# Kernel tuning notes

Measured on AMD Instinct MI355X. Metric: run time of the kernel, lower is better.

The kernel has to match this reference:

```python
import jax, jax.numpy as jnp
import numpy as np

D = 33        # n_vertices
HID = 256     # hidden_features
N_RANKS = 5


def setup_inputs() -> dict:
    key = jax.random.key(0)
    ks = jax.random.split(key, 8)
    img = jax.random.uniform(ks[0], (1, 3, 2160, 3840), dtype=jnp.float32)
    param = jax.random.normal(ks[1], (1, N_RANKS), dtype=jnp.float32) * 0.1

    def lin(k, fan_in, fan_out):
        lim = 1.0 / np.sqrt(fan_in)
        kw, kb = jax.random.split(k)
        W = jax.random.uniform(kw, (fan_in, fan_out), minval=-lim, maxval=lim, dtype=jnp.float32)
        b = jax.random.uniform(kb, (fan_out,), minval=-lim, maxval=lim, dtype=jnp.float32)
        return W, b

    W0, b0 = lin(ks[2], 11, HID)
    W1, b1 = lin(ks[3], HID, HID)
    W2, b2 = lin(ks[4], HID, HID)
    W3, b3 = lin(ks[5], HID, HID)
    W4, b4 = lin(ks[6], HID, 3)
    return dict(img=img, param=param, W0=W0, b0=b0, W1=W1, b1=b1,
                W2=W2, b2=b2, W3=W3, b3=b3, W4=W4, b4=b4)


def _identity_lut_flat():
    # torch: stack(meshgrid(ij), 0)/ (D-1), flip(0), reshape (1,3,D^3)
    v = jnp.arange(D, dtype=jnp.float32)
    g = jnp.stack(jnp.meshgrid(v, v, v, indexing='ij'), axis=0) / (D - 1)
    return g[::-1].reshape(1, 3, -1)  # (1, 3, 35937)


def _nilut(intensity, W0, b0, W1, b1, W2, b2, W3, b3, W4, b4):
    # intensity: (B, N, 8) = [r, g, b, params...]
    inp = jnp.concatenate([intensity, jnp.sort(intensity[..., :3], axis=-1)], axis=-1)  # (B,N,11)
    zero_inp = inp[:1].at[:, :, 3:-3].set(0.0)  # zero the param channels

    def net(x):
        h = jax.nn.relu(x @ W0 + b0)
        h = jnp.tanh(h @ W1 + b1)
        h = jnp.tanh(h @ W2 + b2)
        h = jnp.tanh(h @ W3 + b3)
        return h @ W4 + b4

    return net(inp) - net(zero_inp) + intensity[..., :3]


def _trilinear_lookup(img, luts):
    # img: (B,3,H,W) in [0,1]; luts: (B,3,D,D,D) indexed [c, b_idx, g_idx, r_idx]
    s = img * (D - 1)
    idx = jnp.clip(jnp.floor(s), 0, D - 2).astype(jnp.int32)
    f = s - idx.astype(s.dtype)

    def one(lut_b, idx_b, f_b):
        ir, ig, ib = idx_b[0], idx_b[1], idx_b[2]
        fr, fg, fb = f_b[0], f_b[1], f_b[2]

        def g(db, dg, dr):
            return lut_b[:, ib + db, ig + dg, ir + dr]  # (3,H,W)

        return (g(0, 0, 0) * (1 - fb) * (1 - fg) * (1 - fr)
                + g(0, 0, 1) * (1 - fb) * (1 - fg) * fr
                + g(0, 1, 0) * (1 - fb) * fg * (1 - fr)
                + g(0, 1, 1) * (1 - fb) * fg * fr
                + g(1, 0, 0) * fb * (1 - fg) * (1 - fr)
                + g(1, 0, 1) * fb * (1 - fg) * fr
                + g(1, 1, 0) * fb * fg * (1 - fr)
                + g(1, 1, 1) * fb * fg * fr)

    return jax.vmap(one)(luts, idx, f)


def reference(img, param, W0, b0, W1, b1, W2, b2, W3, b3, W4, b4):
    B = param.shape[0]
    ident = _identity_lut_flat()                              # (1,3,N)
    Nl = ident.shape[2]
    tiled = jnp.broadcast_to(param[:, :, None], (B, N_RANKS, Nl))
    ins = jnp.concatenate([jnp.broadcast_to(ident, (B, 3, Nl)), tiled], axis=1)  # (B,8,N)
    ins = jnp.transpose(ins, (0, 2, 1))                       # (B,N,8)
    luts = _nilut(ins, W0, b0, W1, b1, W2, b2, W3, b3, W4, b4)  # (B,N,3)
    luts = jnp.transpose(luts, (0, 2, 1)).reshape(B, 3, D, D, D)
    img_rep = jnp.broadcast_to(img, (B,) + img.shape[1:])
    return _trilinear_lookup(img_rep, luts)
```

## Files before the change

kernel.cpp:

```cpp
#include <hip/hip_runtime.h>
#include <hip/hip_fp16.h>
#include <math.h>

#define NPTS 35937
#define HID 256
#define TPB 256

typedef __attribute__((ext_vector_type(8))) short short8;
typedef __attribute__((ext_vector_type(4))) float f32x4;

__device__ __forceinline__ float fast_tanh(float x) {
    float e = __expf(2.0f * x);
    return 1.0f - __fdividef(2.0f, e + 1.0f);
}

__device__ __forceinline__ short f2bf(float f) {
    union { float f; unsigned u; } v; v.f = f;
    unsigned r = (v.u + 0x7fffu + ((v.u >> 16) & 1u)) >> 16;
    return (short)r;
}

__device__ __forceinline__ unsigned cvt_pk_bf16(float a, float b) {
    unsigned r;
    asm("v_cvt_pk_bf16_f32 %0, %1, %2" : "=v"(r) : "v"(a), "v"(b));
    return r;
}

#define W1P_OFF 8192
#define W2P_OFF 73728
#define W3P_OFF 139264
#define W4P_OFF 204800
#define LUT_BYTE_OFF 417792
#define CELL_BYTE_OFF 992896

__global__ __launch_bounds__(256) void pack_weights_kernel(
    const float* __restrict__ W0, const float* __restrict__ W1,
    const float* __restrict__ W2, const float* __restrict__ W3,
    const float* __restrict__ W4, short* __restrict__ P)
{
    int id = blockIdx.x * 256 + threadIdx.x;
    if (id >= 26112) return;
    const float* W; int f, NT, KREAL, NROW; long pbase;
    if (id < 1024)       { W = W0; f = id;         NT = 16; KREAL = 11;  NROW = 256; pbase = 0; }
    else if (id < 9216)  { W = W1; f = id - 1024;  NT = 16; KREAL = 256; NROW = 256; pbase = W1P_OFF; }
    else if (id < 17408) { W = W2; f = id - 9216;  NT = 16; KREAL = 256; NROW = 256; pbase = W2P_OFF; }
    else if (id < 25600) { W = W3; f = id - 17408; NT = 16; KREAL = 256; NROW = 256; pbase = W3P_OFF; }
    else                 { W = W4; f = id - 25600; NT = 1;  KREAL = 256; NROW = 3;   pbase = W4P_OFF; }
    int lane = f & 63;
    int tile = f >> 6;
    int nt = tile % NT, kt = tile / NT;
    int n  = nt * 16 + (lane & 15);
    int k0 = kt * 32 + ((lane >> 4) & 3) * 8;
    short v[8];
    #pragma unroll
    for (int j = 0; j < 8; ++j) {
        int k = k0 + j;
        float x = (k < KREAL && n < NROW) ? W[k * NROW + n] : 0.0f;
        v[j] = f2bf(x);
    }
    *(short8*)(P + pbase + (long)f * 8) = *(short8*)v;
}

#define HSTR 264

__global__ __launch_bounds__(256) void nilut_mfma_kernel(
    const float* __restrict__ param, const short* __restrict__ P,
    const float* __restrict__ b0, const float* __restrict__ b1,
    const float* __restrict__ b2, const float* __restrict__ b3,
    const float* __restrict__ b4, float* __restrict__ lut4)
{
    __shared__ short Hs[32][HSTR];
    __shared__ short Is[32][40];
    __shared__ float OB[32][4];

    const int t = threadIdx.x;
    const int pblock = blockIdx.x * 16;
    const int lane = t & 63;
    const int wid  = t >> 6;
    const int lr = lane & 15;
    const int hi = lane >> 4;
    const int k8 = hi * 8;

    if (t < 32) {
        int pn = pblock + (t >> 1);
        if (pn >= NPTS) pn = NPTS - 1;
        int v = t & 1;
        int ii = pn / 1089;
        int rem = pn - ii * 1089;
        int jj = rem / 33;
        int kk = rem - jj * 33;
        float r = kk * (1.0f / 32.0f);
        float g = jj * (1.0f / 32.0f);
        float b = ii * (1.0f / 32.0f);
        float lo = fminf(r, fminf(g, b));
        float hv = fmaxf(r, fmaxf(g, b));
        float mid = r + g + b - lo - hv;
        Is[t][0] = f2bf(r); Is[t][1] = f2bf(g); Is[t][2] = f2bf(b);
        #pragma unroll
        for (int q = 0; q < 5; ++q)
            Is[t][3 + q] = (v == 0) ? f2bf(param[q]) : (short)0;
        Is[t][8] = f2bf(lo); Is[t][9] = f2bf(mid); Is[t][10] = f2bf(hv);
        #pragma unroll
        for (int q = 11; q < 40; ++q) Is[t][q] = (short)0;
    }
    __syncthreads();

    f32x4 acc[2][4];
    const int nbase = wid * 64 + hi * 4;

    {
        #pragma unroll
        for (int c = 0; c < 4; ++c) {
            float4 bv = *(const float4*)(b0 + nbase + c * 16);
            f32x4 in = {bv.x, bv.y, bv.z, bv.w};
            #pragma unroll
            for (int rt = 0; rt < 2; ++rt) acc[rt][c] = in;
        }
        short8 a[2], bfr[4];
        #pragma unroll
        for (int rt = 0; rt < 2; ++rt) a[rt] = *(const short8*)&Is[rt * 16 + lr][k8];
        #pragma unroll
        for (int c = 0; c < 4; ++c)
            bfr[c] = *(const short8*)(P + ((long)(wid * 4 + c) * 64 + lane) * 8);
        #pragma unroll
        for (int rt = 0; rt < 2; ++rt)
            #pragma unroll
            for (int c = 0; c < 4; ++c)
                acc[rt][c] = __builtin_amdgcn_mfma_f32_16x16x32_bf16(bfr[c], a[rt], acc[rt][c], 0, 0, 0);
        #pragma unroll
        for (int rt = 0; rt < 2; ++rt)
            #pragma unroll
            for (int c = 0; c < 4; ++c) {
                uint2 w;
                w.x = cvt_pk_bf16(fmaxf(acc[rt][c][0], 0.0f), fmaxf(acc[rt][c][1], 0.0f));
                w.y = cvt_pk_bf16(fmaxf(acc[rt][c][2], 0.0f), fmaxf(acc[rt][c][3], 0.0f));
                *(uint2*)&Hs[rt * 16 + lr][nbase + c * 16] = w;
            }
    }
    __syncthreads();

    const long loff[3] = {W1P_OFF, W2P_OFF, W3P_OFF};
    const float* bptr[3];
    bptr[0] = b1; bptr[1] = b2; bptr[2] = b3;
    for (int L = 0; L < 3; ++L) {
        const short* WL = P + loff[L];
        const float* bb = bptr[L];
        #pragma unroll
        for (int c = 0; c < 4; ++c) {
            float4 bv = *(const float4*)(bb + nbase + c * 16);
            f32x4 in = {bv.x, bv.y, bv.z, bv.w};
            #pragma unroll
            for (int rt = 0; rt < 2; ++rt) acc[rt][c] = in;
        }
        #pragma unroll
        for (int kt = 0; kt < 8; ++kt) {
            short8 a[2], bfr[4];
            #pragma unroll
            for (int rt = 0; rt < 2; ++rt)
                a[rt] = *(const short8*)&Hs[rt * 16 + lr][kt * 32 + k8];
            #pragma unroll
            for (int c = 0; c < 4; ++c)
                bfr[c] = *(const short8*)(WL + ((long)(kt * 16 + wid * 4 + c) * 64 + lane) * 8);
            #pragma unroll
            for (int rt = 0; rt < 2; ++rt)
                #pragma unroll
                for (int c = 0; c < 4; ++c)
                    acc[rt][c] = __builtin_amdgcn_mfma_f32_16x16x32_bf16(bfr[c], a[rt], acc[rt][c], 0, 0, 0);
        }
        __syncthreads();
        #pragma unroll
        for (int rt = 0; rt < 2; ++rt)
            #pragma unroll
            for (int c = 0; c < 4; ++c) {
                uint2 w;
                w.x = cvt_pk_bf16(fast_tanh(acc[rt][c][0]), fast_tanh(acc[rt][c][1]));
                w.y = cvt_pk_bf16(fast_tanh(acc[rt][c][2]), fast_tanh(acc[rt][c][3]));
                *(uint2*)&Hs[rt * 16 + lr][nbase + c * 16] = w;
            }
        __syncthreads();
    }

    if (wid < 2) {
        float bv = (lr < 3) ? b4[lr] : 0.0f;
        f32x4 a4 = {bv, bv, bv, bv};
        const short* WL = P + W4P_OFF;
        #pragma unroll
        for (int kt = 0; kt < 8; ++kt) {
            short8 a = *(const short8*)&Hs[wid * 16 + lr][kt * 32 + k8];
            short8 b = *(const short8*)(WL + ((long)kt * 64 + lane) * 8);
            a4 = __builtin_amdgcn_mfma_f32_16x16x32_bf16(a, b, a4, 0, 0, 0);
        }
        if (lr < 3) {
            #pragma unroll
            for (int q = 0; q < 4; ++q)
                OB[wid * 16 + hi * 4 + q][lr] = a4[q];
        }
    }
    __syncthreads();

    if (t < 48) {
        int pl = t / 3, c = t - pl * 3;
        int n = pblock + pl;
        if (n < NPTS) {
            int ii = n / 1089;
            int rem = n - ii * 1089;
            int jj = rem / 33;
            int kk = rem - jj * 33;
            float rgb = (c == 0) ? kk * (1.0f / 32.0f)
                      : (c == 1) ? jj * (1.0f / 32.0f)
                                 : ii * (1.0f / 32.0f);
            lut4[n * 4 + c] = OB[2 * pl][c] - OB[2 * pl + 1][c] + rgb;
        }
    }
}

__global__ __launch_bounds__(256) void expand_cells_kernel(
    const float* __restrict__ lut4, __half* __restrict__ cells)
{
    int id = blockIdx.x * 256 + threadIdx.x;
    if (id >= 32768 * 8) return;
    int corner = id & 7;
    int cell   = id >> 3;
    int ir = cell & 31, ig = (cell >> 5) & 31, ib = cell >> 10;
    int dr = corner & 1, dg = (corner >> 1) & 1, db = (corner >> 2) & 1;
    int src = (ib + db) * 1089 + (ig + dg) * 33 + (ir + dr);
    float4 v = *(const float4*)(lut4 + (long)src * 4);
    union { __half h[4]; uint2 u; } pk;
    pk.h[0] = __float2half_rn(v.x);
    pk.h[1] = __float2half_rn(v.y);
    pk.h[2] = __float2half_rn(v.z);
    pk.h[3] = __float2half_rn(0.0f);
    *(uint2*)(cells + (long)cell * 32 + corner * 4) = pk.u;
}

#define LERP(a, b, f) fmaf((f), (b) - (a), (a))

__global__ __launch_bounds__(256) void apply_lut_kernel(
    const float* __restrict__ img, const __half* __restrict__ cells,
    float* __restrict__ out)
{
    const int NP = 2160 * 3840;
    int idx = blockIdx.x * blockDim.x + threadIdx.x;
    int p = idx * 4;
    if (p >= NP) return;

    float4 rv = *(const float4*)(img + p);
    float4 gv = *(const float4*)(img + NP + p);
    float4 bv = *(const float4*)(img + 2 * NP + p);

    float rr[4] = {rv.x, rv.y, rv.z, rv.w};
    float gg[4] = {gv.x, gv.y, gv.z, gv.w};
    float bb[4] = {bv.x, bv.y, bv.z, bv.w};
    float ox[4], oy[4], oz[4];

    #pragma unroll
    for (int u = 0; u < 4; ++u) {
        float sr = rr[u] * 32.0f, sg = gg[u] * 32.0f, sb = bb[u] * 32.0f;
        float fir = fminf(fmaxf(floorf(sr), 0.0f), 31.0f);
        float fig = fminf(fmaxf(floorf(sg), 0.0f), 31.0f);
        float fib = fminf(fmaxf(floorf(sb), 0.0f), 31.0f);
        float fr = sr - fir, fg = sg - fig, fb = sb - fib;
        int ir = (int)fir, ig = (int)fig, ib = (int)fib;

        const short8* cb = (const short8*)(cells + ((long)(ib * 1024 + ig * 32 + ir)) * 32);
        union { short8 s; __half h[8]; } u0, u1, u2, u3;
        u0.s = cb[0]; u1.s = cb[1]; u2.s = cb[2]; u3.s = cb[3];

        float v00[3], v01[3], v10[3], v11[3];
        #pragma unroll
        for (int c = 0; c < 3; ++c) {
            v00[c] = LERP(__half2float(u0.h[c]), __half2float(u0.h[c + 4]), fr);
            v01[c] = LERP(__half2float(u1.h[c]), __half2float(u1.h[c + 4]), fr);
            v10[c] = LERP(__half2float(u2.h[c]), __half2float(u2.h[c + 4]), fr);
            v11[c] = LERP(__half2float(u3.h[c]), __half2float(u3.h[c + 4]), fr);
        }
        ox[u] = LERP(LERP(v00[0], v01[0], fg), LERP(v10[0], v11[0], fg), fb);
        oy[u] = LERP(LERP(v00[1], v01[1], fg), LERP(v10[1], v11[1], fg), fb);
        oz[u] = LERP(LERP(v00[2], v01[2], fg), LERP(v10[2], v11[2], fg), fb);
    }

    *(float4*)(out + p)          = make_float4(ox[0], ox[1], ox[2], ox[3]);
    *(float4*)(out + NP + p)     = make_float4(oy[0], oy[1], oy[2], oy[3]);
    *(float4*)(out + 2 * NP + p) = make_float4(oz[0], oz[1], oz[2], oz[3]);
}

extern "C" void kernel_launch(void* const* d_in, const int* in_sizes, int n_in,
                              void* d_out, int out_size, void* d_ws, size_t ws_size,
                              hipStream_t stream) {
    const float* img   = (const float*)d_in[0];
    const float* param = (const float*)d_in[1];
    const float* W0 = (const float*)d_in[2];
    const float* b0 = (const float*)d_in[3];
    const float* W1 = (const float*)d_in[4];
    const float* b1 = (const float*)d_in[5];
    const float* W2 = (const float*)d_in[6];
    const float* b2 = (const float*)d_in[7];
    const float* W3 = (const float*)d_in[8];
    const float* b3 = (const float*)d_in[9];
    const float* W4 = (const float*)d_in[10];
    const float* b4 = (const float*)d_in[11];

    short*  P     = (short*)d_ws;
    float*  lut4  = (float*)((char*)d_ws + LUT_BYTE_OFF);
    __half* cells = (__half*)((char*)d_ws + CELL_BYTE_OFF);
    float*  out   = (float*)d_out;

    hipLaunchKernelGGL(pack_weights_kernel, dim3(102), dim3(TPB), 0, stream,
                       W0, W1, W2, W3, W4, P);

    int lut_blocks = (NPTS + 15) / 16;
    hipLaunchKernelGGL(nilut_mfma_kernel, dim3(lut_blocks), dim3(TPB), 0, stream,
                       param, P, b0, b1, b2, b3, b4, lut4);

    hipLaunchKernelGGL(expand_cells_kernel, dim3(1024), dim3(TPB), 0, stream,
                       lut4, cells);

    const int NP = 2160 * 3840;
    int apply_blocks = (NP / 4 + TPB - 1) / TPB;
    hipLaunchKernelGGL(apply_lut_kernel, dim3(apply_blocks), dim3(TPB), 0, stream,
                       img, cells, out);
}
```

Baseline: 132.4 us.

## Fuse cell expansion into NILUT kernel and make apply kernel grid-stride with prefetch

The NILUT kernel now scatters each LUT vertex directly as fp16 into the eight cells it belongs to. This removes the intermediate lut4 buffer and the separate expand_cells launch. The apply kernel becomes a persistent grid-stride loop over 2048 blocks that prefetches the next quad's image data while processing the current one. Costs are scattered 8-byte stores from only 16 threads per block, and lower parallelism in the apply stage.

```diff
diff --git a/kernel.cpp b/kernel.cpp
--- a/kernel.cpp
+++ b/kernel.cpp
@@ -30,7 +30,6 @@
 #define W2P_OFF 73728
 #define W3P_OFF 139264
 #define W4P_OFF 204800
-#define LUT_BYTE_OFF 417792
 #define CELL_BYTE_OFF 992896
 
 __global__ __launch_bounds__(256) void pack_weights_kernel(
@@ -67,7 +66,7 @@
     const float* __restrict__ param, const short* __restrict__ P,
     const float* __restrict__ b0, const float* __restrict__ b1,
     const float* __restrict__ b2, const float* __restrict__ b3,
-    const float* __restrict__ b4, float* __restrict__ lut4)
+    const float* __restrict__ b4, __half* __restrict__ cells)
 {
     __shared__ short Hs[32][HSTR];
     __shared__ short Is[32][40];
@@ -198,90 +197,103 @@
     }
     __syncthreads();
 
-    if (t < 48) {
-        int pl = t / 3, c = t - pl * 3;
-        int n = pblock + pl;
+    if (t < 16) {
+        int n = pblock + t;
         if (n < NPTS) {
             int ii = n / 1089;
             int rem = n - ii * 1089;
             int jj = rem / 33;
             int kk = rem - jj * 33;
-            float rgb = (c == 0) ? kk * (1.0f / 32.0f)
-                      : (c == 1) ? jj * (1.0f / 32.0f)
-                                 : ii * (1.0f / 32.0f);
-            lut4[n * 4 + c] = OB[2 * pl][c] - OB[2 * pl + 1][c] + rgb;
-        }
-    }
-}
-
-__global__ __launch_bounds__(256) void expand_cells_kernel(
-    const float* __restrict__ lut4, __half* __restrict__ cells)
+            float vr = OB[2 * t][0] - OB[2 * t + 1][0] + kk * (1.0f / 32.0f);
+            float vg = OB[2 * t][1] - OB[2 * t + 1][1] + jj * (1.0f / 32.0f);
+            float vb = OB[2 * t][2] - OB[2 * t + 1][2] + ii * (1.0f / 32.0f);
+            union { __half h[4]; uint2 u; } pk;
+            pk.h[0] = __float2half_rn(vr);
+            pk.h[1] = __float2half_rn(vg);
+            pk.h[2] = __float2half_rn(vb);
+            pk.h[3] = __float2half_rn(0.0f);
+            #pragma unroll
+            for (int corner = 0; corner < 8; ++corner) {
+                int dr = corner & 1, dg = (corner >> 1) & 1, db = corner >> 2;
+                int cr = kk - dr, cg = jj - dg, cb = ii - db;
+                if ((unsigned)cr < 32u && (unsigned)cg < 32u && (unsigned)cb < 32u) {
+                    long cell = cb * 1024 + cg * 32 + cr;
+                    *(uint2*)(cells + cell * 32 + corner * 4) = pk.u;
+                }
+            }
+        }
+    }
+}
+
+#define LERP(a, b, f) fmaf((f), (b) - (a), (a))
+#define AP_BLOCKS 2048
+#define AP_TPB 256
+
+__device__ __forceinline__ void lut_px(const __half* __restrict__ cells,
+                                       float r, float g, float b,
+                                       float& orr, float& og, float& ob)
 {
-    int id = blockIdx.x * 256 + threadIdx.x;
-    if (id >= 32768 * 8) return;
-    int corner = id & 7;
-    int cell   = id >> 3;
-    int ir = cell & 31, ig = (cell >> 5) & 31, ib = cell >> 10;
-    int dr = corner & 1, dg = (corner >> 1) & 1, db = (corner >> 2) & 1;
-    int src = (ib + db) * 1089 + (ig + dg) * 33 + (ir + dr);
-    float4 v = *(const float4*)(lut4 + (long)src * 4);
-    union { __half h[4]; uint2 u; } pk;
-    pk.h[0] = __float2half_rn(v.x);
-    pk.h[1] = __float2half_rn(v.y);
-    pk.h[2] = __float2half_rn(v.z);
-    pk.h[3] = __float2half_rn(0.0f);
-    *(uint2*)(cells + (long)cell * 32 + corner * 4) = pk.u;
-}
-
-#define LERP(a, b, f) fmaf((f), (b) - (a), (a))
+    float sr = r * 32.0f, sg = g * 32.0f, sb = b * 32.0f;
+    float fir = fminf(fmaxf(floorf(sr), 0.0f), 31.0f);
+    float fig = fminf(fmaxf(floorf(sg), 0.0f), 31.0f);
+    float fib = fminf(fmaxf(floorf(sb), 0.0f), 31.0f);
+    float fr = sr - fir, fg = sg - fig, fb = sb - fib;
+    int ir = (int)fir, ig = (int)fig, ib = (int)fib;
+
+    const short8* cb = (const short8*)(cells + ((long)(ib * 1024 + ig * 32 + ir)) * 32);
+    union { short8 s; __half h[8]; } u0, u1, u2, u3;
+    u0.s = cb[0]; u1.s = cb[1]; u2.s = cb[2]; u3.s = cb[3];
+
+    float v00[3], v01[3], v10[3], v11[3];
+    #pragma unroll
+    for (int c = 0; c < 3; ++c) {
+        v00[c] = LERP(__half2float(u0.h[c]), __half2float(u0.h[c + 4]), fr);
+        v01[c] = LERP(__half2float(u1.h[c]), __half2float(u1.h[c + 4]), fr);
+        v10[c] = LERP(__half2float(u2.h[c]), __half2float(u2.h[c + 4]), fr);
+        v11[c] = LERP(__half2float(u3.h[c]), __half2float(u3.h[c + 4]), fr);
+    }
+    orr = LERP(LERP(v00[0], v01[0], fg), LERP(v10[0], v11[0], fg), fb);
+    og  = LERP(LERP(v00[1], v01[1], fg), LERP(v10[1], v11[1], fg), fb);
+    ob  = LERP(LERP(v00[2], v01[2], fg), LERP(v10[2], v11[2], fg), fb);
+}
 
 __global__ __launch_bounds__(256) void apply_lut_kernel(
     const float* __restrict__ img, const __half* __restrict__ cells,
     float* __restrict__ out)
 {
     const int NP = 2160 * 3840;
-    int idx = blockIdx.x * blockDim.x + threadIdx.x;
-    int p = idx * 4;
-    if (p >= NP) return;
-
-    float4 rv = *(const float4*)(img + p);
-    float4 gv = *(const float4*)(img + NP + p);
-    float4 bv = *(const float4*)(img + 2 * NP + p);
-
-    float rr[4] = {rv.x, rv.y, rv.z, rv.w};
-    float gg[4] = {gv.x, gv.y, gv.z, gv.w};
-    float bb[4] = {bv.x, bv.y, bv.z, bv.w};
-    float ox[4], oy[4], oz[4];
-
-    #pragma unroll
-    for (int u = 0; u < 4; ++u) {
-        float sr = rr[u] * 32.0f, sg = gg[u] * 32.0f, sb = bb[u] * 32.0f;
-        float fir = fminf(fmaxf(floorf(sr), 0.0f), 31.0f);
-        float fig = fminf(fmaxf(floorf(sg), 0.0f), 31.0f);
-        float fib = fminf(fmaxf(floorf(sb), 0.0f), 31.0f);
-        float fr = sr - fir, fg = sg - fig, fb = sb - fib;
-        int ir = (int)fir, ig = (int)fig, ib = (int)fib;
-
-        const short8* cb = (const short8*)(cells + ((long)(ib * 1024 + ig * 32 + ir)) * 32);
-        union { short8 s; __half h[8]; } u0, u1, u2, u3;
-        u0.s = cb[0]; u1.s = cb[1]; u2.s = cb[2]; u3.s = cb[3];
-
-        float v00[3], v01[3], v10[3], v11[3];
-        #pragma unroll
-        for (int c = 0; c < 3; ++c) {
-            v00[c] = LERP(__half2float(u0.h[c]), __half2float(u0.h[c + 4]), fr);
-            v01[c] = LERP(__half2float(u1.h[c]), __half2float(u1.h[c + 4]), fr);
-            v10[c] = LERP(__half2float(u2.h[c]), __half2float(u2.h[c + 4]), fr);
-            v11[c] = LERP(__half2float(u3.h[c]), __half2float(u3.h[c + 4]), fr);
-        }
-        ox[u] = LERP(LERP(v00[0], v01[0], fg), LERP(v10[0], v11[0], fg), fb);
-        oy[u] = LERP(LERP(v00[1], v01[1], fg), LERP(v10[1], v11[1], fg), fb);
-        oz[u] = LERP(LERP(v00[2], v01[2], fg), LERP(v10[2], v11[2], fg), fb);
-    }
-
-    *(float4*)(out + p)          = make_float4(ox[0], ox[1], ox[2], ox[3]);
-    *(float4*)(out + NP + p)     = make_float4(oy[0], oy[1], oy[2], oy[3]);
-    *(float4*)(out + 2 * NP + p) = make_float4(oz[0], oz[1], oz[2], oz[3]);
+    const int NQ = NP / 4;
+    const int stride = AP_BLOCKS * AP_TPB;
+    int q = blockIdx.x * AP_TPB + threadIdx.x;
+    if (q >= NQ) return;
+
+    float4 rv = *(const float4*)(img + q * 4);
+    float4 gv = *(const float4*)(img + NP + q * 4);
+    float4 bv = *(const float4*)(img + 2 * NP + q * 4);
+
+    while (true) {
+        int qn = q + stride;
+        int qc = (qn < NQ) ? qn : q;
+        float4 rv2 = *(const float4*)(img + qc * 4);
+        float4 gv2 = *(const float4*)(img + NP + qc * 4);
+        float4 bv2 = *(const float4*)(img + 2 * NP + qc * 4);
+
+        float rr[4] = {rv.x, rv.y, rv.z, rv.w};
+        float gg[4] = {gv.x, gv.y, gv.z, gv.w};
+        float bb[4] = {bv.x, bv.y, bv.z, bv.w};
+        float ox[4], oy[4], oz[4];
+        #pragma unroll
+        for (int u = 0; u < 4; ++u)
+            lut_px(cells, rr[u], gg[u], bb[u], ox[u], oy[u], oz[u]);
+
+        int p = q * 4;
+        *(float4*)(out + p)          = make_float4(ox[0], ox[1], ox[2], ox[3]);
+        *(float4*)(out + NP + p)     = make_float4(oy[0], oy[1], oy[2], oy[3]);
+        *(float4*)(out + 2 * NP + p) = make_float4(oz[0], oz[1], oz[2], oz[3]);
+
+        if (qn >= NQ) break;
+        q = qn; rv = rv2; gv = gv2; bv = bv2;
+    }
 }
 
 extern "C" void kernel_launch(void* const* d_in, const int* in_sizes, int n_in,
@@ -301,7 +313,6 @@
     const float* b4 = (const float*)d_in[11];
 
     short*  P     = (short*)d_ws;
-    float*  lut4  = (float*)((char*)d_ws + LUT_BYTE_OFF);
     __half* cells = (__half*)((char*)d_ws + CELL_BYTE_OFF);
     float*  out   = (float*)d_out;
 
@@ -310,13 +321,8 @@
 
     int lut_blocks = (NPTS + 15) / 16;
     hipLaunchKernelGGL(nilut_mfma_kernel, dim3(lut_blocks), dim3(TPB), 0, stream,
-                       param, P, b0, b1, b2, b3, b4, lut4);
-
-    hipLaunchKernelGGL(expand_cells_kernel, dim3(1024), dim3(TPB), 0, stream,
-                       lut4, cells);
-
-    const int NP = 2160 * 3840;
-    int apply_blocks = (NP / 4 + TPB - 1) / TPB;
-    hipLaunchKernelGGL(apply_lut_kernel, dim3(apply_blocks), dim3(TPB), 0, stream,
+                       param, P, b0, b1, b2, b3, b4, cells);
+
+    hipLaunchKernelGGL(apply_lut_kernel, dim3(AP_BLOCKS), dim3(AP_TPB), 0, stream,
                        img, cells, out);
 }
```

Result: slower. 145.7 us (+10.0%).
